# Kernel tuning notes

Measured on AMD Instinct MI355X. Metric: run time of the kernel, lower is better.

Reference implementation:

```python
import jax, jax.numpy as jnp
import numpy as np


def _bilinear(x, py, px):
    # x: [B,C,H,W]; py,px: [B,K,Ho,Wo] fractional sample coords (zero pad outside)
    B, C, H, W = x.shape
    K, Ho, Wo = py.shape[1], py.shape[2], py.shape[3]
    xf = x.reshape(B, C, H * W)
    y0 = jnp.floor(py)
    x0 = jnp.floor(px)

    def gather(yi, xi):
        valid = (yi >= 0) & (yi <= H - 1) & (xi >= 0) & (xi <= W - 1)
        yc = jnp.clip(yi, 0, H - 1).astype(jnp.int32)
        xc = jnp.clip(xi, 0, W - 1).astype(jnp.int32)
        idx = (yc * W + xc).reshape(B, 1, -1)  # [B,1,K*Ho*Wo]
        v = jnp.take_along_axis(xf, idx, axis=2)  # [B,C,K*Ho*Wo]
        return v * valid.reshape(B, 1, -1)

    wy1 = (py - y0).reshape(B, 1, -1)
    wx1 = (px - x0).reshape(B, 1, -1)
    wy0 = 1.0 - wy1
    wx0 = 1.0 - wx1
    v = (gather(y0, x0) * (wy0 * wx0)
         + gather(y0, x0 + 1) * (wy0 * wx1)
         + gather(y0 + 1, x0) * (wy1 * wx0)
         + gather(y0 + 1, x0 + 1) * (wy1 * wx1))
    return v.reshape(B, C, K, Ho, Wo)


def _deform_merge(x, w_off, b_off, w_def, gamma, beta):
    B, C, H, W = x.shape
    Co = w_def.shape[0]
    K, stride = 4, 2  # 2x2 kernel
    Ho, Wo = H // 2, W // 2
    # offset-predicting conv (same k/s/p as deform conv): [B, 2K, Ho, Wo]
    off = jax.lax.conv_general_dilated(x, w_off, (stride, stride), 'VALID')
    off = off + b_off[None, :, None, None]
    off = off.reshape(B, K, 2, Ho, Wo)  # (dy, dx) per kernel tap
    ky = jnp.arange(K) // 2
    kx = jnp.arange(K) % 2
    base_y = (jnp.arange(Ho) * stride)[None, None, :, None] + ky[None, :, None, None]
    base_x = (jnp.arange(Wo) * stride)[None, None, None, :] + kx[None, :, None, None]
    py = base_y.astype(x.dtype) + off[:, :, 0]
    px = base_x.astype(x.dtype) + off[:, :, 1]
    sampled = _bilinear(x, py, px)  # [B,C,K,Ho,Wo]
    y = jnp.einsum('bckhw,ock->bohw', sampled, w_def.reshape(Co, C, K))
    # BatchNorm2d (training-mode batch stats, eps=1e-5) + exact GELU
    mu = y.mean(axis=(0, 2, 3), keepdims=True)
    var = y.var(axis=(0, 2, 3), keepdims=True)
    yn = (y - mu) * jax.lax.rsqrt(var + 1e-5)
    yn = yn * gamma[None, :, None, None] + beta[None, :, None, None]
    yg = jax.nn.gelu(yn, approximate=False)
    return yg.reshape(B, Co, Ho * Wo).transpose(0, 2, 1)  # [B, L/4, Co]


def setup_inputs() -> dict:
    key = jax.random.key(0)
    k0, k1, k2 = jax.random.split(key, 3)
    B, C, H, W, Co = 16, 96, 112, 112, 192
    x = jax.random.normal(k0, (B, C, H, W), jnp.float32)
    # conv_offset: 2*kh*kw = 8 output channels (zero-init in mmcv; small random here)
    w_off = jax.random.normal(k1, (8, C, 2, 2), jnp.float32) * 0.01
    b_off = jnp.zeros((8,), jnp.float32)
    w_def = jax.random.normal(k2, (Co, C, 2, 2), jnp.float32) * (1.0 / np.sqrt(C * 4))
    gamma = jnp.ones((Co,), jnp.float32)
    beta = jnp.zeros((Co,), jnp.float32)
    return {"x": x, "h": H, "w": W, "w_off": w_off, "b_off": b_off,
            "w_def": w_def, "gamma": gamma, "beta": beta}


def reference(x, h, w, w_off, b_off, w_def, gamma, beta):
    assert x.shape[2] == h and x.shape[3] == w
    return _deform_merge(x, w_off, b_off, w_def, gamma, beta)
```

## Files before the change

kernel.cpp:

```cpp
#include <hip/hip_runtime.h>
#include <math.h>

#define BB 16
#define CC 96
#define HH 112
#define WW 112
#define HO 56
#define WO 56
#define LL (HO*WO)
#define CO 192
#define CKD 384
#define NPIX (BB*LL)
#define PADROW 388

#define WS_SSUM  16
#define WS_SSQS  208
#define WS_SCALE 400
#define WS_SHIFT 592
#define WS_B_OFF 4096
#define B_ELEMS  73728

typedef short bf16x8 __attribute__((ext_vector_type(8)));
typedef float f32x4  __attribute__((ext_vector_type(4)));

__device__ __forceinline__ void split8(const float4 a0, const float4 a1,
                                       bf16x8& hi, bf16x8& lo)
{
    float f[8] = {a0.x, a0.y, a0.z, a0.w, a1.x, a1.y, a1.z, a1.w};
    #pragma unroll
    for (int j = 0; j < 8; ++j) {
        unsigned bits = __float_as_uint(f[j]);
        float fh = __uint_as_float(bits & 0xFFFF0000u);
        float fl = f[j] - fh;
        hi[j] = (short)(bits >> 16);
        lo[j] = (short)(__float_as_uint(fl) >> 16);
    }
}

__global__ void k_zero(float* __restrict__ ws) {
    int t = threadIdx.x;
    if (t < 384) ws[WS_SSUM + t] = 0.f;
}

__global__ void k_prep(const float* __restrict__ w_def,
                       unsigned short* __restrict__ bhi,
                       unsigned short* __restrict__ blo)
{
    int t = blockIdx.x * 256 + threadIdx.x;
    if (t >= 12 * 12 * 64) return;
    int ln  = t & 63;
    int ks  = (t >> 6) % 12;
    int ntg = t / (64 * 12);
    int n  = ntg * 16 + (ln & 15);
    int k0 = ks * 32 + (ln >> 4) * 8;
    const float* wp = w_def + (size_t)n * CKD + k0;
    #pragma unroll
    for (int j = 0; j < 8; ++j) {
        float f = wp[j];
        unsigned bits = __float_as_uint(f);
        float fh = __uint_as_float(bits & 0xFFFF0000u);
        float fl = f - fh;
        bhi[t * 8 + j] = (unsigned short)(bits >> 16);
        blo[t * 8 + j] = (unsigned short)(__float_as_uint(fl) >> 16);
    }
}

template<bool PREP>
__global__ __launch_bounds__(256) void k_main(
    const float* __restrict__ x,
    const float* __restrict__ w_off,
    const float* __restrict__ b_off,
    const float* __restrict__ w_def,
    const unsigned short* __restrict__ bhi,
    const unsigned short* __restrict__ blo,
    float* __restrict__ yout,
    float* __restrict__ ws)
{
    __shared__ float sm[32 * PADROW];
    __shared__ float soff[32 * 8];
    const int tid = threadIdx.x;
    const int b  = blockIdx.y;
    const int l0 = blockIdx.x * 32;

    const int pair = tid >> 1;
    const int half = tid & 1;
    const int pix = pair >> 2;
    const int k   = pair & 3;
    const int l   = l0 + pix;
    const int oy = l / WO, ox = l % WO;
    const int iy = oy * 2, ix = ox * 2;

    {
        const int och = 2 * k + half;
        float d = b_off[och];
        const float* xb = x + ((size_t)b * CC) * (HH * WW) + (size_t)iy * WW + ix;
        const float* wb = w_off + (size_t)och * (CC * 4);
        for (int c = 0; c < CC; ++c) {
            const float* xp = xb + (size_t)c * (HH * WW);
            float4 a = *(const float4*)(wb + c * 4);
            d += xp[0] * a.x + xp[1] * a.y + xp[WW] * a.z + xp[WW + 1] * a.w;
        }
        soff[pix * 8 + och] = d;
    }
    __syncthreads();

    {
        const int ky = k >> 1, kx = k & 1;
        float fy = (float)(iy + ky) + soff[pix * 8 + 2 * k];
        float fx = (float)(ix + kx) + soff[pix * 8 + 2 * k + 1];
        float y0f = floorf(fy), x0f = floorf(fx);
        int y0 = (int)y0f, x0 = (int)x0f;
        float wy1 = fy - y0f, wx1 = fx - x0f;
        float wy0 = 1.f - wy1, wx0 = 1.f - wx1;
        int y1 = y0 + 1, x1 = x0 + 1;
        bool vy0 = (y0 >= 0) && (y0 <= HH - 1);
        bool vy1 = (y1 >= 0) && (y1 <= HH - 1);
        bool vx0 = (x0 >= 0) && (x0 <= WW - 1);
        bool vx1 = (x1 >= 0) && (x1 <= WW - 1);
        int cy0 = min(max(y0, 0), HH - 1), cy1 = min(max(y1, 0), HH - 1);
        int cx0 = min(max(x0, 0), WW - 1), cx1 = min(max(x1, 0), WW - 1);
        float w00 = (vy0 && vx0) ? wy0 * wx0 : 0.f;
        float w01 = (vy0 && vx1) ? wy0 * wx1 : 0.f;
        float w10 = (vy1 && vx0) ? wy1 * wx0 : 0.f;
        float w11 = (vy1 && vx1) ? wy1 * wx1 : 0.f;
        int i00 = cy0 * WW + cx0, i01 = cy0 * WW + cx1;
        int i10 = cy1 * WW + cx0, i11 = cy1 * WW + cx1;
        const int cbeg = half * 48;
        const float* xc = x + (size_t)b * CC * (HH * WW) + (size_t)cbeg * (HH * WW);
        float* dst = &sm[pix * PADROW + k];
        for (int c = 0; c < 48; ++c) {
            float v = w00 * xc[i00] + w01 * xc[i01]
                    + w10 * xc[i10] + w11 * xc[i11];
            dst[(cbeg + c) * 4] = v;
            xc += HH * WW;
        }
    }
    __syncthreads();

    const int ln = tid & 63;
    const int w  = tid >> 6;
    const int row0 = ln & 15;
    const int kg   = ln >> 4;

    f32x4 acc[2][3];
    #pragma unroll
    for (int mt = 0; mt < 2; ++mt)
        #pragma unroll
        for (int nt = 0; nt < 3; ++nt)
            acc[mt][nt] = (f32x4){0.f, 0.f, 0.f, 0.f};

    for (int ks = 0; ks < 12; ++ks) {
        bf16x8 ahi[2], alo[2];
        #pragma unroll
        for (int mt = 0; mt < 2; ++mt) {
            const float* ap = &sm[(mt * 16 + row0) * PADROW + ks * 32 + kg * 8];
            float4 a0 = *(const float4*)ap;
            float4 a1 = *(const float4*)(ap + 4);
            split8(a0, a1, ahi[mt], alo[mt]);
        }
        #pragma unroll
        for (int nt = 0; nt < 3; ++nt) {
            bf16x8 vbh, vbl;
            if (PREP) {
                size_t idx = ((size_t)(((w * 3 + nt) * 12 + ks) * 64) + ln) * 8;
                vbh = *(const bf16x8*)(bhi + idx);
                vbl = *(const bf16x8*)(blo + idx);
            } else {
                const float* wp = w_def + (size_t)(w * 48 + nt * 16 + row0) * CKD
                                + ks * 32 + kg * 8;
                float4 b0 = *(const float4*)wp;
                float4 b1 = *(const float4*)(wp + 4);
                split8(b0, b1, vbh, vbl);
            }
            #pragma unroll
            for (int mt = 0; mt < 2; ++mt) {
                acc[mt][nt] = __builtin_amdgcn_mfma_f32_16x16x32_bf16(ahi[mt], vbh, acc[mt][nt], 0, 0, 0);
                acc[mt][nt] = __builtin_amdgcn_mfma_f32_16x16x32_bf16(ahi[mt], vbl, acc[mt][nt], 0, 0, 0);
                acc[mt][nt] = __builtin_amdgcn_mfma_f32_16x16x32_bf16(alo[mt], vbh, acc[mt][nt], 0, 0, 0);
            }
        }
    }
    __syncthreads();

    float* ys = sm;
    #pragma unroll
    for (int mt = 0; mt < 2; ++mt)
        #pragma unroll
        for (int nt = 0; nt < 3; ++nt)
            #pragma unroll
            for (int r = 0; r < 4; ++r) {
                int pp = mt * 16 + kg * 4 + r;
                int o  = w * 48 + nt * 16 + row0;
                ys[pp * 193 + o] = acc[mt][nt][r];
            }
    __syncthreads();

    if (tid < CO) {
        float s = 0.f, q = 0.f;
        #pragma unroll 8
        for (int p = 0; p < 32; ++p) {
            float v = ys[p * 193 + tid];
            s += v; q += v * v;
        }
        atomicAdd(&ws[WS_SSUM + tid], s);
        atomicAdd(&ws[WS_SSQS + tid], q);
    }

    size_t base = ((size_t)b * LL + l0) * CO;
    for (int i = tid; i < 32 * CO; i += 256) {
        int pp = i / CO, o = i % CO;
        yout[base + i] = ys[pp * 193 + o];
    }
}

__global__ void k_stats(const float* __restrict__ gamma,
                        const float* __restrict__ beta,
                        float* __restrict__ ws)
{
    int o = threadIdx.x;
    if (o < CO) {
        float n = (float)NPIX;
        float mu = ws[WS_SSUM + o] / n;
        float var = ws[WS_SSQS + o] / n - mu * mu;
        float sc = gamma[o] * rsqrtf(fmaxf(var, 0.f) + 1e-5f);
        ws[WS_SCALE + o] = sc;
        ws[WS_SHIFT + o] = beta[o] - mu * sc;
    }
}

__global__ __launch_bounds__(256) void k_bn_gelu(
    float* __restrict__ out,
    const float* __restrict__ ws)
{
    long long gid = (long long)blockIdx.x * 256 + threadIdx.x;
    long long i4 = gid * 4;
    if (i4 >= (long long)NPIX * CO) return;
    int o0 = (int)(i4 % CO);
    float4* p = (float4*)(out + i4);
    float4 v = *p;
    float f[4] = { v.x, v.y, v.z, v.w };
    #pragma unroll
    for (int j = 0; j < 4; ++j) {
        float z = ws[WS_SCALE + o0 + j] * f[j] + ws[WS_SHIFT + o0 + j];
        f[j] = 0.5f * z * (1.f + erff(z * 0.70710678118654752f));
    }
    v.x = f[0]; v.y = f[1]; v.z = f[2]; v.w = f[3];
    *p = v;
}

extern "C" void kernel_launch(void* const* d_in, const int* in_sizes, int n_in,
                              void* d_out, int out_size, void* d_ws, size_t ws_size,
                              hipStream_t stream)
{
    const float *x = nullptr, *w_off = nullptr, *b_off = nullptr;
    const float *w_def = nullptr, *gamma = nullptr, *beta = nullptr;
    for (int i = 0; i < n_in; ++i) {
        int s = in_sizes[i];
        if      (s == 19267584) x     = (const float*)d_in[i];
        else if (s == 3072)     w_off = (const float*)d_in[i];
        else if (s == 8)        b_off = (const float*)d_in[i];
        else if (s == 73728)    w_def = (const float*)d_in[i];
        else if (s == 192) { if (!gamma) gamma = (const float*)d_in[i];
                             else        beta  = (const float*)d_in[i]; }
    }
    if (!x || !w_off || !b_off || !w_def || !gamma || !beta) {
        x = (const float*)d_in[0]; w_off = (const float*)d_in[3];
        b_off = (const float*)d_in[4]; w_def = (const float*)d_in[5];
        gamma = (const float*)d_in[6]; beta = (const float*)d_in[7];
    }

    float* ws = (float*)d_ws;
    float* out = (float*)d_out;

    unsigned short* bhi = (unsigned short*)((char*)d_ws + WS_B_OFF);
    unsigned short* blo = bhi + B_ELEMS;
    bool prep = ws_size >= (size_t)(WS_B_OFF + 2 * B_ELEMS * sizeof(unsigned short));

    k_zero<<<1, 384, 0, stream>>>(ws);
    if (prep) {
        k_prep<<<36, 256, 0, stream>>>(w_def, bhi, blo);
        k_main<true><<<dim3(LL/32, BB), 256, 0, stream>>>(x, w_off, b_off, w_def, bhi, blo, out, ws);
    } else {
        k_main<false><<<dim3(LL/32, BB), 256, 0, stream>>>(x, w_off, b_off, w_def, bhi, blo, out, ws);
    }
    k_stats<<<1, 256, 0, stream>>>(gamma, beta, ws);
    k_bn_gelu<<<dim3((int)(((long long)NPIX*CO/4 + 255) / 256)), 256, 0, stream>>>(out, ws);
}
```

Before: 331.9 us.

## Tile main kernel by half output rows with shared-memory input windows

Result: no change. 337.5 us (+1.7%).

```diff
diff --git a/kernel.cpp b/kernel.cpp
--- a/kernel.cpp
+++ b/kernel.cpp
@@ -11,12 +11,16 @@
 #define CO 192
 #define CKD 384
 #define NPIX (BB*LL)
-#define PADROW 388
+
+#define TPX 28
+#define CHK 8
+#define NCHUNK 12
+#define WROWS 6
+#define WCOLS 64
+#define APAD 40
 
 #define WS_SSUM  16
 #define WS_SSQS  208
-#define WS_SCALE 400
-#define WS_SHIFT 592
 #define WS_B_OFF 4096
 #define B_ELEMS  73728
 
@@ -44,8 +48,10 @@
 
 __global__ void k_prep(const float* __restrict__ w_def,
                        unsigned short* __restrict__ bhi,
-                       unsigned short* __restrict__ blo)
-{
+                       unsigned short* __restrict__ blo,
+                       float* __restrict__ ws)
+{
+    if (blockIdx.x == 0 && threadIdx.x < 384) ws[WS_SSUM + threadIdx.x] = 0.f;
     int t = blockIdx.x * 256 + threadIdx.x;
     if (t >= 12 * 12 * 64) return;
     int ln  = t & 63;
@@ -66,7 +72,7 @@
 }
 
 template<bool PREP>
-__global__ __launch_bounds__(256) void k_main(
+__global__ __launch_bounds__(256, 4) void k_main(
     const float* __restrict__ x,
     const float* __restrict__ w_off,
     const float* __restrict__ b_off,
@@ -76,71 +82,59 @@
     float* __restrict__ yout,
     float* __restrict__ ws)
 {
-    __shared__ float sm[32 * PADROW];
-    __shared__ float soff[32 * 8];
+    __shared__ float win[CHK * WROWS * WCOLS];
+    __shared__ unsigned short smAh[32 * APAD];
+    __shared__ unsigned short smAl[32 * APAD];
+    __shared__ float soff[TPX * 8];
+
     const int tid = threadIdx.x;
     const int b  = blockIdx.y;
-    const int l0 = blockIdx.x * 32;
-
-    const int pair = tid >> 1;
-    const int half = tid & 1;
-    const int pix = pair >> 2;
-    const int k   = pair & 3;
-    const int l   = l0 + pix;
-    const int oy = l / WO, ox = l % WO;
-    const int iy = oy * 2, ix = ox * 2;
-
-    {
-        const int och = 2 * k + half;
-        float d = b_off[och];
-        const float* xb = x + ((size_t)b * CC) * (HH * WW) + (size_t)iy * WW + ix;
-        const float* wb = w_off + (size_t)och * (CC * 4);
-        for (int c = 0; c < CC; ++c) {
-            const float* xp = xb + (size_t)c * (HH * WW);
-            float4 a = *(const float4*)(wb + c * 4);
-            d += xp[0] * a.x + xp[1] * a.y + xp[WW] * a.z + xp[WW + 1] * a.w;
-        }
-        soff[pix * 8 + och] = d;
-    }
-    __syncthreads();
-
-    {
-        const int ky = k >> 1, kx = k & 1;
-        float fy = (float)(iy + ky) + soff[pix * 8 + 2 * k];
-        float fx = (float)(ix + kx) + soff[pix * 8 + 2 * k + 1];
-        float y0f = floorf(fy), x0f = floorf(fx);
-        int y0 = (int)y0f, x0 = (int)x0f;
-        float wy1 = fy - y0f, wx1 = fx - x0f;
-        float wy0 = 1.f - wy1, wx0 = 1.f - wx1;
-        int y1 = y0 + 1, x1 = x0 + 1;
-        bool vy0 = (y0 >= 0) && (y0 <= HH - 1);
-        bool vy1 = (y1 >= 0) && (y1 <= HH - 1);
-        bool vx0 = (x0 >= 0) && (x0 <= WW - 1);
-        bool vx1 = (x1 >= 0) && (x1 <= WW - 1);
-        int cy0 = min(max(y0, 0), HH - 1), cy1 = min(max(y1, 0), HH - 1);
-        int cx0 = min(max(x0, 0), WW - 1), cx1 = min(max(x1, 0), WW - 1);
-        float w00 = (vy0 && vx0) ? wy0 * wx0 : 0.f;
-        float w01 = (vy0 && vx1) ? wy0 * wx1 : 0.f;
-        float w10 = (vy1 && vx0) ? wy1 * wx0 : 0.f;
-        float w11 = (vy1 && vx1) ? wy1 * wx1 : 0.f;
-        int i00 = cy0 * WW + cx0, i01 = cy0 * WW + cx1;
-        int i10 = cy1 * WW + cx0, i11 = cy1 * WW + cx1;
-        const int cbeg = half * 48;
-        const float* xc = x + (size_t)b * CC * (HH * WW) + (size_t)cbeg * (HH * WW);
-        float* dst = &sm[pix * PADROW + k];
-        for (int c = 0; c < 48; ++c) {
-            float v = w00 * xc[i00] + w01 * xc[i01]
-                    + w10 * xc[i10] + w11 * xc[i11];
-            dst[(cbeg + c) * 4] = v;
-            xc += HH * WW;
-        }
-    }
-    __syncthreads();
-
+    const int bx = blockIdx.x;
+    const int oy  = bx >> 1;
+    const int ox0 = (bx & 1) * TPX;
+    const int iy  = oy * 2;
+    const int ix0 = ox0 * 2;
     const int ln = tid & 63;
     const int w  = tid >> 6;
+
+    float dacc = 0.f;
+    const int cpix = tid >> 3;
+    const int coch = tid & 7;
+    const int spair = tid / 14;
+    const int sq    = tid % 14;
+    for (int ch = 0; ch < NCHUNK; ++ch) {
+        __syncthreads();
+        if (tid < 224) {
+            int c = spair >> 1, r = spair & 1;
+            const float* src = x + (((size_t)(b * CC + ch * CHK + c) * HH) + iy + r) * WW + ix0 + sq * 4;
+            *(float4*)&win[(c * 2 + r) * 56 + sq * 4] = *(const float4*)src;
+        }
+        __syncthreads();
+        if (tid < 224) {
+            const float* wb = w_off + (size_t)coch * (CC * 4) + ch * CHK * 4;
+            #pragma unroll
+            for (int c = 0; c < CHK; ++c) {
+                float2 t0 = *(const float2*)&win[(c * 2 + 0) * 56 + 2 * cpix];
+                float2 t1 = *(const float2*)&win[(c * 2 + 1) * 56 + 2 * cpix];
+                float4 a = *(const float4*)(wb + c * 4);
+                dacc += t0.x * a.x + t0.y * a.y + t1.x * a.z + t1.y * a.w;
+            }
+        }
+    }
+    if (tid < 224) soff[cpix * 8 + coch] = dacc + b_off[coch];
+    if (tid < 128) {
+        int rr = 28 + (tid >> 5), cc = tid & 31;
+        smAh[rr * APAD + cc] = 0;
+        smAl[rr * APAD + cc] = 0;
+    }
+
     const int row0 = ln & 15;
     const int kg   = ln >> 4;
+    const int skk = tid & 31;
+    const int sc  = skk >> 2;
+    const int sk  = skk & 3;
+    const int sky = sk >> 1, skx = sk & 1;
+    const int wr0 = iy - 2, wc0 = ix0 - 4;
 
     f32x4 acc[2][3];
     #pragma unroll
@@ -149,91 +143,154 @@
         for (int nt = 0; nt < 3; ++nt)
             acc[mt][nt] = (f32x4){0.f, 0.f, 0.f, 0.f};
 
-    for (int ks = 0; ks < 12; ++ks) {
-        bf16x8 ahi[2], alo[2];
+    for (int ch = 0; ch < NCHUNK; ++ch) {
+        __syncthreads();
+        #pragma unroll
+        for (int j = 0; j < 3; ++j) {
+            int li = tid + 256 * j;
+            int cg = li & 15, pr = li >> 4;
+            int r = pr % 6, c = pr / 6;
+            int gr = min(max(wr0 + r, 0), HH - 1);
+            int gc0 = wc0 + cg * 4;
+            const float* src = x + (((size_t)(b * CC + ch * CHK + c) * HH) + gr) * WW;
+            float4 v;
+            if (gc0 >= 0 && gc0 <= WW - 4) {
+                v = *(const float4*)(src + gc0);
+            } else {
+                v.x = src[min(max(gc0 + 0, 0), WW - 1)];
+                v.y = src[min(max(gc0 + 1, 0), WW - 1)];
+                v.z = src[min(max(gc0 + 2, 0), WW - 1)];
+                v.w = src[min(max(gc0 + 3, 0), WW - 1)];
+            }
+            *(float4*)&win[(c * WROWS + r) * WCOLS + cg * 4] = v;
+        }
+        __syncthreads();
+        {
+            const float* xc = x + ((size_t)(b * CC + ch * CHK + sc) * HH) * WW;
+            const float* wchan = &win[(sc * WROWS) * WCOLS];
+            #pragma unroll
+            for (int j = 0; j < 4; ++j) {
+                if (j < 3 || tid < 128) {
+                    int pix = (tid >> 5) + 8 * j;
+                    float2 so = *(const float2*)&soff[pix * 8 + 2 * sk];
+                    float fy = (float)(iy + sky) + so.x;
+                    float fx = (float)(ix0 + 2 * pix + skx) + so.y;
+                    float y0f = floorf(fy), x0f = floorf(fx);
+                    int y0 = (int)y0f, x0 = (int)x0f;
+                    float wy1 = fy - y0f, wx1 = fx - x0f;
+                    float wy0 = 1.f - wy1, wx0 = 1.f - wx1;
+                    int y1 = y0 + 1, x1 = x0 + 1;
+                    bool vy0 = (y0 >= 0) && (y0 <= HH - 1);
+                    bool vy1 = (y1 >= 0) && (y1 <= HH - 1);
+                    bool vx0 = (x0 >= 0) && (x0 <= WW - 1);
+                    bool vx1 = (x1 >= 0) && (x1 <= WW - 1);
+                    int cy0 = min(max(y0, 0), HH - 1), cy1 = min(max(y1, 0), HH - 1);
+                    int cx0 = min(max(x0, 0), WW - 1), cx1 = min(max(x1, 0), WW - 1);
+                    float w00 = (vy0 && vx0) ? wy0 * wx0 : 0.f;
+                    float w01 = (vy0 && vx1) ? wy0 * wx1 : 0.f;
+                    float w10 = (vy1 && vx0) ? wy1 * wx0 : 0.f;
+                    float w11 = (vy1 && vx1) ? wy1 * wx1 : 0.f;
+                    int ry0 = cy0 - wr0, ry1 = cy1 - wr0;
+                    int rx0 = cx0 - wc0, rx1 = cx1 - wc0;
+                    bool inw = ((unsigned)ry0 <= (unsigned)(WROWS - 1)) &&
+                               ((unsigned)ry1 <= (unsigned)(WROWS - 1)) &&
+                               ((unsigned)rx0 <= (unsigned)(WCOLS - 1)) &&
+                               ((unsigned)rx1 <= (unsigned)(WCOLS - 1));
+                    float v;
+                    if (inw) {
+                        v = w00 * wchan[ry0 * WCOLS + rx0] + w01 * wchan[ry0 * WCOLS + rx1]
+                          + w10 * wchan[ry1 * WCOLS + rx0] + w11 * wchan[ry1 * WCOLS + rx1];
+                    } else {
+                        v = w00 * xc[cy0 * WW + cx0] + w01 * xc[cy0 * WW + cx1]
+                          + w10 * xc[cy1 * WW + cx0] + w11 * xc[cy1 * WW + cx1];
+                    }
+                    unsigned u = __float_as_uint(v);
+                    float fh = __uint_as_float(u & 0xFFFF0000u);
+                    smAh[pix * APAD + skk] = (unsigned short)(u >> 16);
+                    smAl[pix * APAD + skk] = (unsigned short)(__float_as_uint(v - fh) >> 16);
+                }
+            }
+        }
+        __syncthreads();
+        bf16x8 ah[2], al[2];
         #pragma unroll
         for (int mt = 0; mt < 2; ++mt) {
-            const float* ap = &sm[(mt * 16 + row0) * PADROW + ks * 32 + kg * 8];
-            float4 a0 = *(const float4*)ap;
-            float4 a1 = *(const float4*)(ap + 4);
-            split8(a0, a1, ahi[mt], alo[mt]);
+            ah[mt] = *(const bf16x8*)&smAh[(mt * 16 + row0) * APAD + kg * 8];
+            al[mt] = *(const bf16x8*)&smAl[(mt * 16 + row0) * APAD + kg * 8];
         }
         #pragma unroll
         for (int nt = 0; nt < 3; ++nt) {
-            bf16x8 vbh, vbl;
+            bf16x8 bh, bl;
             if (PREP) {
-                size_t idx = ((size_t)(((w * 3 + nt) * 12 + ks) * 64) + ln) * 8;
-                vbh = *(const bf16x8*)(bhi + idx);
-                vbl = *(const bf16x8*)(blo + idx);
+                size_t idx = ((size_t)(((w * 3 + nt) * 12 + ch) * 64) + ln) * 8;
+                bh = *(const bf16x8*)(bhi + idx);
+                bl = *(const bf16x8*)(blo + idx);
             } else {
                 const float* wp = w_def + (size_t)(w * 48 + nt * 16 + row0) * CKD
-                                + ks * 32 + kg * 8;
+                                + ch * 32 + kg * 8;
                 float4 b0 = *(const float4*)wp;
                 float4 b1 = *(const float4*)(wp + 4);
-                split8(b0, b1, vbh, vbl);
+                split8(b0, b1, bh, bl);
             }
             #pragma unroll
             for (int mt = 0; mt < 2; ++mt) {
-                acc[mt][nt] = __builtin_amdgcn_mfma_f32_16x16x32_bf16(ahi[mt], vbh, acc[mt][nt], 0, 0, 0);
-                acc[mt][nt] = __builtin_amdgcn_mfma_f32_16x16x32_bf16(ahi[mt], vbl, acc[mt][nt], 0, 0, 0);
-                acc[mt][nt] = __builtin_amdgcn_mfma_f32_16x16x32_bf16(alo[mt], vbh, acc[mt][nt], 0, 0, 0);
-            }
-        }
-    }
-    __syncthreads();
-
-    float* ys = sm;
-    #pragma unroll
-    for (int mt = 0; mt < 2; ++mt)
-        #pragma unroll
-        for (int nt = 0; nt < 3; ++nt)
+                acc[mt][nt] = __builtin_amdgcn_mfma_f32_16x16x32_bf16(ah[mt], bh, acc[mt][nt], 0, 0, 0);
+                acc[mt][nt] = __builtin_amdgcn_mfma_f32_16x16x32_bf16(ah[mt], bl, acc[mt][nt], 0, 0, 0);
+                acc[mt][nt] = __builtin_amdgcn_mfma_f32_16x16x32_bf16(al[mt], bh, acc[mt][nt], 0, 0, 0);
+            }
+        }
+    }
+
+    #pragma unroll
+    for (int nt = 0; nt < 3; ++nt) {
+        float s = 0.f, q = 0.f;
+        #pragma unroll
+        for (int mt = 0; mt < 2; ++mt)
             #pragma unroll
             for (int r = 0; r < 4; ++r) {
-                int pp = mt * 16 + kg * 4 + r;
-                int o  = w * 48 + nt * 16 + row0;
-                ys[pp * 193 + o] = acc[mt][nt][r];
-            }
-    __syncthreads();
-
-    if (tid < CO) {
-        float s = 0.f, q = 0.f;
-        #pragma unroll 8
-        for (int p = 0; p < 32; ++p) {
-            float v = ys[p * 193 + tid];
-            s += v; q += v * v;
-        }
-        atomicAdd(&ws[WS_SSUM + tid], s);
-        atomicAdd(&ws[WS_SSQS + tid], q);
-    }
-
-    size_t base = ((size_t)b * LL + l0) * CO;
-    for (int i = tid; i < 32 * CO; i += 256) {
-        int pp = i / CO, o = i % CO;
-        yout[base + i] = ys[pp * 193 + o];
-    }
-}
-
-__global__ void k_stats(const float* __restrict__ gamma,
-                        const float* __restrict__ beta,
-                        float* __restrict__ ws)
-{
-    int o = threadIdx.x;
-    if (o < CO) {
-        float n = (float)NPIX;
-        float mu = ws[WS_SSUM + o] / n;
-        float var = ws[WS_SSQS + o] / n - mu * mu;
-        float sc = gamma[o] * rsqrtf(fmaxf(var, 0.f) + 1e-5f);
-        ws[WS_SCALE + o] = sc;
-        ws[WS_SHIFT + o] = beta[o] - mu * sc;
-    }
+                float v = acc[mt][nt][r];
+                s += v; q += v * v;
+            }
+        s += __shfl_xor(s, 16); s += __shfl_xor(s, 32);
+        q += __shfl_xor(q, 16); q += __shfl_xor(q, 32);
+        if (ln < 16) {
+            atomicAdd(&ws[WS_SSUM + w * 48 + nt * 16 + ln], s);
+            atomicAdd(&ws[WS_SSQS + w * 48 + nt * 16 + ln], q);
+        }
+    }
+    size_t obase = (size_t)b * LL + (size_t)oy * WO + ox0;
+    #pragma unroll
+    for (int mt = 0; mt < 2; ++mt)
+        #pragma unroll
+        for (int r = 0; r < 4; ++r) {
+            int pp = mt * 16 + kg * 4 + r;
+            if (pp < TPX) {
+                float* dst = yout + (obase + pp) * CO + w * 48 + row0;
+                dst[0]  = acc[mt][0][r];
+                dst[16] = acc[mt][1][r];
+                dst[32] = acc[mt][2][r];
+            }
+        }
 }
 
 __global__ __launch_bounds__(256) void k_bn_gelu(
     float* __restrict__ out,
+    const float* __restrict__ gamma,
+    const float* __restrict__ beta,
     const float* __restrict__ ws)
 {
-    long long gid = (long long)blockIdx.x * 256 + threadIdx.x;
-    long long i4 = gid * 4;
+    __shared__ float ssc[CO], ssh[CO];
+    int t = threadIdx.x;
+    if (t < CO) {
+        float n = (float)NPIX;
+        float mu = ws[WS_SSUM + t] / n;
+        float var = ws[WS_SSQS + t] / n - mu * mu;
+        float sc = gamma[t] * rsqrtf(fmaxf(var, 0.f) + 1e-5f);
+        ssc[t] = sc;
+        ssh[t] = beta[t] - mu * sc;
+    }
+    __syncthreads();
+    long long i4 = ((long long)blockIdx.x * 256 + t) * 4;
     if (i4 >= (long long)NPIX * CO) return;
     int o0 = (int)(i4 % CO);
     float4* p = (float4*)(out + i4);
@@ -241,7 +298,7 @@
     float f[4] = { v.x, v.y, v.z, v.w };
     #pragma unroll
     for (int j = 0; j < 4; ++j) {
-        float z = ws[WS_SCALE + o0 + j] * f[j] + ws[WS_SHIFT + o0 + j];
+        float z = ssc[o0 + j] * f[j] + ssh[o0 + j];
         f[j] = 0.5f * z * (1.f + erff(z * 0.70710678118654752f));
     }
     v.x = f[0]; v.y = f[1]; v.z = f[2]; v.w = f[3];
@@ -276,13 +333,12 @@
     unsigned short* blo = bhi + B_ELEMS;
     bool prep = ws_size >= (size_t)(WS_B_OFF + 2 * B_ELEMS * sizeof(unsigned short));
 
-    k_zero<<<1, 384, 0, stream>>>(ws);
     if (prep) {
-        k_prep<<<36, 256, 0, stream>>>(w_def, bhi, blo);
-        k_main<true><<<dim3(LL/32, BB), 256, 0, stream>>>(x, w_off, b_off, w_def, bhi, blo, out, ws);
+        k_prep<<<36, 256, 0, stream>>>(w_def, bhi, blo, ws);
+        k_main<true><<<dim3(112, BB), 256, 0, stream>>>(x, w_off, b_off, w_def, bhi, blo, out, ws);
     } else {
-        k_main<false><<<dim3(LL/32, BB), 256, 0, stream>>>(x, w_off, b_off, w_def, bhi, blo, out, ws);
-    }
-    k_stats<<<1, 256, 0, stream>>>(gamma, beta, ws);
-    k_bn_gelu<<<dim3((int)(((long long)NPIX*CO/4 + 255) / 256)), 256, 0, stream>>>(out, ws);
-}
+        k_zero<<<1, 384, 0, stream>>>(ws);
+        k_main<false><<<dim3(112, BB), 256, 0, stream>>>(x, w_off, b_off, w_def, bhi, blo, out, ws);
+    }
+    k_bn_gelu<<<dim3((int)(((long long)NPIX*CO/4 + 255) / 256)), 256, 0, stream>>>(out, gamma, beta, ws);
+}
```
